# Performance work log

Hardware: AMD Instinct MI355X
Metric: run time of the kernel (lower is better)

Reference implementation:

```python
import jax, jax.numpy as jnp
import numpy as np

VS = 0.4
PC = (-75.2, -75.2, -2.0, 75.2, 75.2, 4.0)
K = 32            # max_points_per_voxel (stage 1)
K2 = 5            # max_points_per_voxel (stage 2)
MAXV = 50000      # max_num_voxels
GAMMA = 1.1
SENT = 1_000_000  # coord sentinel for empty voxel slots


def _voxelize(pts, valid, vx, vy, vz, max_vox, max_ppv):
    """Fixed-capacity voxelization (mimics spconv PointToVoxel).
    pts: [N,F] (xyz in first 3 cols); valid: [N] bool.
    Returns voxels [max_vox, max_ppv, F], coords_xy [max_vox,2] int32 (SENT for empty), num_points [max_vox]."""
    N, F = pts.shape
    gx = int(round((PC[3] - PC[0]) / vx))
    gy = int(round((PC[4] - PC[1]) / vy))
    gz = int(round((PC[5] - PC[2]) / vz))
    cx = jnp.floor((pts[:, 0] - PC[0]) / vx).astype(jnp.int32)
    cy = jnp.floor((pts[:, 1] - PC[1]) / vy).astype(jnp.int32)
    cz = jnp.floor((pts[:, 2] - PC[2]) / vz).astype(jnp.int32)
    inb = valid & (cx >= 0) & (cx < gx) & (cy >= 0) & (cy < gy) & (cz >= 0) & (cz < gz)
    BIG = gx * gy * gz
    vid = jnp.where(inb, (cz * gy + cy) * gx + cx, BIG)
    order = jnp.argsort(vid)  # stable sort groups points by voxel
    sid = vid[order]
    spts = pts[order]
    first = jnp.searchsorted(sid, sid, side='left')
    last = jnp.searchsorted(sid, sid, side='right')
    rank = jnp.arange(N, dtype=jnp.int32) - first.astype(jnp.int32)
    is_first = (rank == 0) & (sid < BIG)
    slot_all = jnp.cumsum(is_first.astype(jnp.int32)) - 1
    slot = slot_all[first]
    keep = (sid < BIG) & (rank < max_ppv) & (slot < max_vox)
    s = jnp.where(keep, slot, max_vox)
    r = jnp.where(keep, rank, 0)
    voxels = jnp.zeros((max_vox + 1, max_ppv, F), pts.dtype).at[s, r].set(spts)[:max_vox]
    sf = jnp.where(is_first & (slot_all < max_vox), slot_all, max_vox)
    cnt = jnp.where(is_first, jnp.minimum(last - first, max_ppv), 0).astype(jnp.int32)
    nump = jnp.zeros((max_vox + 1,), jnp.int32).at[sf].set(cnt)[:max_vox]
    cxy = jnp.stack([cx[order], cy[order]], -1)
    coords = jnp.full((max_vox + 1, 2), SENT, jnp.int32).at[sf].set(cxy)[:max_vox]
    return voxels, coords, nump


def _forward(points, trajectory_rois, backward_rois, valid_length, batch_size, num_sample):
    B, T, R, _ = trajectory_rois.shape
    pc_start = jnp.array(PC[:2], jnp.float32)
    mixed_xy = (trajectory_rois[..., :2] + backward_rois[..., :2]) * 0.5
    rois_xy = jnp.where(valid_length[..., None], mixed_xy, backward_rois[..., :2])
    rois = jnp.concatenate([rois_xy, backward_rois[..., 2:]], -1)
    per_batch = []
    for bs in range(B):
        per_frame = []
        for t in range(T):
            valid = (points[:, 0] == bs) & (jnp.abs(points[:, 5] - t * 0.1) < 0.001)
            pts = points[:, 1:6]  # (x,y,z,feat,time) = 5 point features
            boxes = rois[bs, t]   # [R,7]
            # ---- stage 1: coarse voxelization (full z column) ----
            vox, coords, nump = _voxelize(pts, valid, VS, VS, PC[5] - PC[2], MAXV, K)
            q = jnp.floor((boxes[:, :2] - pc_start) / VS)
            rad = jnp.ceil(jnp.linalg.norm(boxes[:, 3:5] / 2, axis=-1) * GAMMA / VS)
            dist = jnp.abs(q[:, None, :] - coords[None].astype(jnp.float32))  # [R,V,2]
            vmask = jnp.any(jnp.all(dist < rad[:, None, None], -1), 0)        # [V]
            npm = jnp.where(vmask, nump, 0)
            kvalid = (jnp.arange(K)[None, :] < npm[:, None]).reshape(-1)
            kpts = vox.reshape(-1, 5)
            # ---- stage 2: fine voxelization of key points ----
            vox1, coords1, _ = _voxelize(kpts, kvalid, VS / 2, VS / 2, VS / 2, MAXV, K2)
            q1 = jnp.floor((boxes[:, :2] - pc_start) / (VS / 2))
            dist1 = jnp.abs(q1[:, None, :] - coords1[None].astype(jnp.float32))  # [R,V1,2]
            vmask1 = jnp.all(dist1 < (rad * 2)[:, None, None], -1)               # [R,V1]
            _, sidx = jax.lax.top_k(vmask1.astype(jnp.float32), num_sample)      # [R,S]
            sv = vox1[sidx]                                   # [R,S,K2,F]
            sv = sv.transpose(0, 2, 1, 3).reshape(R, K2 * num_sample, 5)
            cur_r = jnp.linalg.norm(boxes[:, 3:5] / 2, axis=-1) * GAMMA
            pm = ((sv[:, :, :2] - boxes[:, None, :2]) ** 2).sum(-1) < cur_r[:, None] ** 2
            pm = pm & (sv[:, :, 2] <= (boxes[:, 2] + boxes[:, 5] * 0.6)[:, None])
            smask, sidx2 = jax.lax.top_k(pm.astype(jnp.float32), num_sample)
            sp = jnp.take_along_axis(sv, sidx2[:, :, None], axis=1)  # [R,S,5]
            sp = jnp.where(smask[:, :, None] > 0, sp, 0.0)
            per_frame.append(sp)
        per_batch.append(jnp.stack(per_frame))  # [T,R,S,5]
    res = jnp.stack(per_batch)                   # [B,T,R,S,5]
    return res.transpose(0, 2, 1, 3, 4).reshape(B, R, T * num_sample, 5)


def setup_inputs() -> dict:
    key = jax.random.key(0)
    k = jax.random.split(key, 10)
    N, B, T, R = 240000, 2, 4, 128
    bs = jax.random.randint(k[0], (N,), 0, B).astype(jnp.float32)
    frame = jax.random.randint(k[1], (N,), 0, T).astype(jnp.float32)
    x = jax.random.uniform(k[2], (N,), minval=-74.0, maxval=74.0)
    y = jax.random.uniform(k[3], (N,), minval=-74.0, maxval=74.0)
    z = jax.random.uniform(k[4], (N,), minval=-2.0, maxval=4.0)
    inten = jax.random.uniform(k[5], (N,))
    points = jnp.stack([bs, x, y, z, inten, frame * 0.1], -1)
    xy = jax.random.uniform(k[6], (B, T, R, 2), minval=-60.0, maxval=60.0)
    zc = jax.random.uniform(k[7], (B, T, R, 1), minval=-1.0, maxval=1.0)
    dims = jax.random.uniform(k[8], (B, T, R, 3), minval=1.0, maxval=5.0)
    yaw = jax.random.uniform(k[9], (B, T, R, 1), minval=-3.14, maxval=3.14)
    trajectory_rois = jnp.concatenate([xy, zc, dims, yaw], -1)
    backward_rois = trajectory_rois.at[..., :2].add(
        0.5 * jax.random.normal(jax.random.fold_in(key, 1), (B, T, R, 2)))
    valid_length = jax.random.randint(jax.random.fold_in(key, 2), (B, T, R), 0, 2).astype(bool)
    return {"points": points, "trajectory_rois": trajectory_rois,
            "backward_rois": backward_rois, "valid_length": valid_length,
            "batch_size": 2, "num_sample": 32}


def reference(points, trajectory_rois, backward_rois, valid_length, batch_size, num_sample):
    return _forward(points, trajectory_rois, backward_rois, valid_length, batch_size, num_sample)
```

## Files before the change

### kernel.cpp

```cpp
#include <hip/hip_runtime.h>

typedef unsigned int u32;
typedef unsigned long long u64;

#define BB 2
#define TT 4
#define NF 8
#define RR 128
#define NSAMP 32
#define KK2 5
#define GX1 376
#define GY1 376
#define GX2 752
#define GY2 752
#define GZ2 30
#define WPF 530160
#define RBW 12
#define NMAXP 262144
#define MAXROWS 1536
#define RPT 6
#define HCAP (1u << 19)
#define HMASK (HCAP - 1u)
#define EMPTYW 0xFFFFFFFFu
#define NOVID 0xFFFFFFFFu
#define NLOW 64
#define CW 8

#define PCX (-75.2f)
#define PCY (-75.2f)
#define PCZ (-2.0f)
#define VS1 0.4f
#define VSH 0.2f
#define VZ1 6.0f

__global__ void k_init(const float* traj, const float* back, const unsigned char* vlb,
                       u32* boxp, u32* z0, u32 n0, u32* f2, u32 n2)
{
    u32 tid = blockIdx.x * blockDim.x + threadIdx.x;
    u32 stride = gridDim.x * blockDim.x;
    if (tid < NF * RR) {
        int i = (int)tid;
        bool isU8 = false;
        for (int k = 1; k < 64; k++)
            if ((k & 3) && vlb[k]) isU8 = true;
        bool vl = isU8 ? (vlb[i] != 0) : (((const int*)vlb)[i] != 0);
        const float* tb = traj + i * 7;
        const float* bb = back + i * 7;
        float bx = vl ? (tb[0] + bb[0]) * 0.5f : bb[0];
        float by = vl ? (tb[1] + bb[1]) * 0.5f : bb[1];
        float bz = bb[2], dx = bb[3], dy = bb[4], dz = bb[5];
        float hx = dx * 0.5f, hy = dy * 0.5f;
        float r0 = sqrtf(hx * hx + hy * hy);
        float radf = ceilf(r0 * 1.1f / 0.4f);
        float curr = r0 * 1.1f;
        u32* bp = boxp + i * 12;
        bp[0] = __float_as_uint(bx);
        bp[1] = __float_as_uint(by);
        bp[2] = __float_as_uint(curr * curr);
        bp[3] = __float_as_uint(bz + dz * 0.6f);
        bp[4] = (u32)(int)floorf((bx - PCX) / VS1);
        bp[5] = (u32)(int)floorf((by - PCY) / VS1);
        bp[6] = (u32)(int)radf;
        bp[7] = (u32)(int)floorf((bx - PCX) / VSH);
        bp[8] = (u32)(int)floorf((by - PCY) / VSH);
        bp[9] = (u32)(2 * (int)radf);
    }
    uint4 zz = make_uint4(0u, 0u, 0u, 0u);
    uint4 fv = make_uint4(~0u, ~0u, ~0u, ~0u);
    for (u32 i = tid; i < n0; i += stride) ((uint4*)z0)[i] = zz;
    for (u32 i = tid; i < n2; i += stride) ((uint4*)f2)[i] = fv;
}

__global__ void k_raster(const u32* boxp, u32* roibm)
{
    int tid = blockIdx.x * blockDim.x + threadIdx.x;
    if (tid >= NF * RR) return;
    const u32* bp = boxp + tid * 12;
    int f = tid / RR;
    int Qx = (int)bp[4], Qy = (int)bp[5], ir = (int)bp[6];
    int xlo = Qx - ir + 1; if (xlo < 0) xlo = 0;
    int xhi = Qx + ir - 1; if (xhi > GX1 - 1) xhi = GX1 - 1;
    int ylo = Qy - ir + 1; if (ylo < 0) ylo = 0;
    int yhi = Qy + ir - 1; if (yhi > GY1 - 1) yhi = GY1 - 1;
    if (xlo > xhi || ylo > yhi) return;
    int w0 = xlo >> 5, w1 = xhi >> 5;
    for (int cy = ylo; cy <= yhi; cy++) {
        u32* row = roibm + (size_t)f * (GY1 * RBW) + cy * RBW;
        for (int w = w0; w <= w1; w++) {
            int lo = xlo - (w << 5); if (lo < 0) lo = 0;
            int hi = xhi - (w << 5); if (hi > 31) hi = 31;
            u32 m = (hi == 31 ? 0xFFFFFFFFu : ((1u << (hi + 1)) - 1u)) & ~((1u << lo) - 1u);
            atomicOr(&row[w], m);
        }
    }
}

__global__ void k_keep(const float* P, int n, const u32* roibm,
                       u32* bitmap, u32* tabk, u32* tabs)
{
    int i = blockIdx.x * blockDim.x + threadIdx.x;
    if (i >= n) return;
    const float* p = P + (size_t)i * 6;
    float bsf = p[0], x = p[1], y = p[2], z = p[3], tt = p[5];
    int b = (int)bsf;
    int t = (int)floorf(tt * 10.0f + 0.5f);
    if (!(bsf == (float)b && b >= 0 && b < BB && t >= 0 && t < TT &&
          fabsf(tt - 0.1f * (float)t) < 0.001f)) return;
    float fx = floorf((x - PCX) / VS1);
    float fy = floorf((y - PCY) / VS1);
    float fz = floorf((z - PCZ) / VZ1);
    if (!(fx >= 0.f && fx < (float)GX1 && fy >= 0.f && fy < (float)GY1 && fz == 0.f)) return;
    u32 f = (u32)(b * TT + t);
    u32 cx = (u32)fx, cy = (u32)fy;
    u32 bit = (roibm[(size_t)f * (GY1 * RBW) + cy * RBW + (cx >> 5)] >> (cx & 31)) & 1u;
    if (!bit) return;
    float fx2 = floorf((x - PCX) / VSH);
    float fy2 = floorf((y - PCY) / VSH);
    float fz2 = floorf((z - PCZ) / VSH);
    if (!(fx2 >= 0.f && fx2 < (float)GX2 && fy2 >= 0.f && fy2 < (float)GY2 &&
          fz2 >= 0.f && fz2 < (float)GZ2)) return;
    u32 vid = ((u32)fz2 * GY2 + (u32)fy2) * GX2 + (u32)fx2;
    u32 pk = (f << 25) | vid;
    atomicOr(&bitmap[f * WPF + (vid >> 5)], 1u << (vid & 31));
    u32 idx = ((pk * 2654435761u) >> 13) & HMASK;
    while (true) {
        u32 old = atomicCAS(&tabk[idx], EMPTYW, pk);
        if (old == EMPTYW || old == pk) break;
        idx = (idx + 1u) & HMASK;
    }
    u32* arr = tabs + (size_t)idx * KK2;
    u32 val = (u32)i;
    #pragma unroll
    for (int j = 0; j < KK2; j++) {
        u32 old = atomicMin(&arr[j], val);
        if (old == EMPTYW) break;
        val = old > val ? old : val;
    }
}

__global__ void __launch_bounds__(256) k_lowvid(const u32* bitmap, u32* lowvids)
{
    __shared__ u32 out_sh[NLOW];
    __shared__ u32 cnt_sh;
    __shared__ u32 wsum_sh[4];
    int f = blockIdx.x, tid = threadIdx.x;
    int lane = tid & 63, wid = tid >> 6;
    const u32* bmf = bitmap + (size_t)f * WPF;
    if (tid == 0) cnt_sh = 0;
    __syncthreads();
    for (u32 base = 0; base < (u32)WPF; base += 256 * CW) {
        u32 w[CW];
        u32 pc = 0;
        u32 tb = base + (u32)tid * CW;
        if (tb + CW <= (u32)WPF) {
            uint4 a = *(const uint4*)(bmf + tb);
            uint4 c4 = *(const uint4*)(bmf + tb + 4);
            w[0] = a.x; w[1] = a.y; w[2] = a.z; w[3] = a.w;
            w[4] = c4.x; w[5] = c4.y; w[6] = c4.z; w[7] = c4.w;
        } else {
            #pragma unroll
            for (u32 e = 0; e < CW; e++) w[e] = (tb + e < (u32)WPF) ? bmf[tb + e] : 0u;
        }
        #pragma unroll
        for (u32 e = 0; e < CW; e++) pc += (u32)__popc(w[e]);
        u32 ws = pc;
        #pragma unroll
        for (int off = 1; off < 64; off <<= 1) {
            u32 y = __shfl_up(ws, off, 64);
            if (lane >= off) ws += y;
        }
        if (lane == 63) wsum_sh[wid] = ws;
        __syncthreads();
        u32 w0 = wsum_sh[0], w1 = wsum_sh[1], w2 = wsum_sh[2], w3 = wsum_sh[3];
        u32 wexcl = (wid > 0 ? w0 : 0u) + (wid > 1 ? w1 : 0u) + (wid > 2 ? w2 : 0u);
        u32 excl = cnt_sh + wexcl + ws - pc;
        u32 totadd = w0 + w1 + w2 + w3;
        if (excl < NLOW && pc) {
            u32 c = excl;
            #pragma unroll
            for (u32 e = 0; e < CW; e++) {
                u32 ww = w[e];
                while (ww && c < NLOW) {
                    u32 b = (u32)__ffs(ww) - 1u;
                    out_sh[c++] = ((tb + e) << 5) | b;
                    ww &= ww - 1u;
                }
            }
        }
        __syncthreads();
        if (tid == 0) {
            u32 nc = cnt_sh + totadd;
            cnt_sh = nc > (u32)NLOW ? (u32)NLOW : nc;
        }
        __syncthreads();
        if (cnt_sh >= (u32)NLOW) break;
    }
    u32 c = cnt_sh;
    for (int e = tid; e < NLOW; e += 256)
        lowvids[f * NLOW + e] = ((u32)e < c) ? out_sh[e] : NOVID;
}

__global__ void __launch_bounds__(256) k_output(const float* P, const u32* boxp,
    const u32* bitmap, const u32* lowvids, const u32* tabk, const u32* tabs, float* out)
{
    __shared__ u32 rpref_s[MAXROWS];
    __shared__ u32 ssum[256];
    __shared__ u32 sidx[NSAMP];
    __shared__ float feat[KK2 * NSAMP][5];
    __shared__ u32 pmf[KK2 * NSAMP];
    __shared__ int sel[NSAMP];
    __shared__ int nsel_s;
    __shared__ u32 M_s;

    int bid = blockIdx.x, tid = threadIdx.x;
    int f = bid / RR, r = bid % RR;
    int b = f / TT, t = f % TT;
    const u32* bp = boxp + bid * 12;
    float bx = __uint_as_float(bp[0]);
    float by = __uint_as_float(bp[1]);
    float cr2 = __uint_as_float(bp[2]);
    float zmax = __uint_as_float(bp[3]);
    int Q1x = (int)bp[7], Q1y = (int)bp[8], irad2 = (int)bp[9];

    const u32* bmf = bitmap + (size_t)f * WPF;

    int cxlo = Q1x - irad2 + 1; if (cxlo < 0) cxlo = 0;
    int cxhi = Q1x + irad2 - 1; if (cxhi > GX2 - 1) cxhi = GX2 - 1;
    int cylo = Q1y - irad2 + 1; if (cylo < 0) cylo = 0;
    int cyhi = Q1y + irad2 - 1; if (cyhi > GY2 - 1) cyhi = GY2 - 1;
    int ny = cyhi - cylo + 1;
    int nrows = (cxlo <= cxhi && cylo <= cyhi) ? GZ2 * ny : 0;
    if (nrows > MAXROWS) nrows = MAXROWS;

    u32 myrpref[RPT];
    u32 lsum = 0;
    #pragma unroll
    for (int e = 0; e < RPT; e++) {
        int ri = tid * RPT + e;
        myrpref[e] = lsum;
        if (ri < nrows) {
            int cz = ri / ny, cy = cylo + (ri - cz * ny);
            u32 vlo = ((u32)cz * GY2 + (u32)cy) * GX2 + (u32)cxlo;
            u32 vhi = vlo + (u32)(cxhi - cxlo);
            u32 gwlo = vlo >> 5, gwhi = vhi >> 5;
            u32 c = 0;
            for (u32 gw = gwlo; gw <= gwhi; gw++) {
                u32 w = bmf[gw];
                u32 lob = (gw == gwlo) ? (vlo & 31u) : 0u;
                u32 hib = (gw == gwhi) ? (vhi & 31u) : 31u;
                u32 m = (hib == 31u ? 0xFFFFFFFFu : ((1u << (hib + 1)) - 1u)) & ~((1u << lob) - 1u);
                c += (u32)__popc(w & m);
            }
            lsum += c;
        }
    }
    ssum[tid] = lsum;
    __syncthreads();
    for (int off = 1; off < 256; off <<= 1) {
        u32 y = (tid >= off) ? ssum[tid - off] : 0;
        __syncthreads();
        ssum[tid] += y;
        __syncthreads();
    }
    u32 texcl = ssum[tid] - lsum;
    if (tid == 255) M_s = ssum[255];
    #pragma unroll
    for (int e = 0; e < RPT; e++) {
        int ri = tid * RPT + e;
        if (ri < MAXROWS) rpref_s[ri] = texcl + myrpref[e];
    }
    __syncthreads();

    u32 M = M_s;
    int nt = (int)(M < (u32)NSAMP ? M : (u32)NSAMP);
    if (tid < nt) {
        int lo = 0, hi = nrows - 1;
        while (lo < hi) { int m = (lo + hi + 1) >> 1; if (rpref_s[m] <= (u32)tid) lo = m; else hi = m - 1; }
        u32 rem = (u32)tid - rpref_s[lo];
        int cz = lo / ny, cy = cylo + (lo - cz * ny);
        u32 vlo = ((u32)cz * GY2 + (u32)cy) * GX2 + (u32)cxlo;
        u32 vhi = vlo + (u32)(cxhi - cxlo);
        u32 gwlo = vlo >> 5, gwhi = vhi >> 5;
        u32 vsel = NOVID;
        for (u32 gw = gwlo; gw <= gwhi; gw++) {
            u32 w = bmf[gw];
            u32 lob = (gw == gwlo) ? (vlo & 31u) : 0u;
            u32 hib = (gw == gwhi) ? (vhi & 31u) : 31u;
            u32 m = (hib == 31u ? 0xFFFFFFFFu : ((1u << (hib + 1)) - 1u)) & ~((1u << lob) - 1u);
            u32 wm = w & m;
            u32 pc = (u32)__popc(wm);
            if (rem < pc) {
                for (u32 k = 0; k < rem; k++) wm &= wm - 1u;
                u32 bit = (u32)__ffs(wm) - 1u;
                vsel = (gw << 5) | bit;
                break;
            }
            rem -= pc;
        }
        sidx[tid] = vsel;
    }
    __syncthreads();
    if (tid == 0) {
        const u32* lv = lowvids + f * NLOW;
        int c = nt, p = 0, q = 0;
        while (c < NSAMP) {
            u32 cand = (q < NLOW) ? lv[q] : NOVID;
            if (cand == NOVID) { sidx[c++] = NOVID; continue; }
            if (p < nt && sidx[p] == cand) { p++; q++; continue; }
            sidx[c++] = cand; q++;
        }
    }
    __syncthreads();

    for (int j2 = tid; j2 < KK2 * NSAMP; j2 += 256) {
        int s = j2 / KK2, k2 = j2 - s * KK2;
        int j = k2 * NSAMP + s;
        u32 vid = sidx[s];
        float px = 0.f, py = 0.f, pz = 0.f, pi = 0.f, pt = 0.f;
        if (vid != NOVID) {
            u32 pk = ((u32)f << 25) | vid;
            u32 idx = ((pk * 2654435761u) >> 13) & HMASK;
            u32 key;
            while (true) {
                key = tabk[idx];
                if (key == pk || key == EMPTYW) break;
                idx = (idx + 1u) & HMASK;
            }
            if (key == pk) {
                u32 pidx = tabs[(size_t)idx * KK2 + k2];
                if (pidx != EMPTYW) {
                    const float* p = P + (size_t)pidx * 6;
                    px = p[1]; py = p[2]; pz = p[3]; pi = p[4]; pt = p[5];
                }
            }
        }
        feat[j][0] = px; feat[j][1] = py; feat[j][2] = pz; feat[j][3] = pi; feat[j][4] = pt;
        float ex = px - bx, ey = py - by;
        pmf[j] = (ex * ex + ey * ey < cr2 && pz <= zmax) ? 1u : 0u;
    }
    __syncthreads();

    if (tid == 0) {
        int c = 0;
        for (int j = 0; j < KK2 * NSAMP && c < NSAMP; j++)
            if (pmf[j]) sel[c++] = j;
        nsel_s = c;
    }
    __syncthreads();

    int obase = ((b * RR + r) * (TT * NSAMP) + t * NSAMP) * 5;
    for (int w = tid; w < NSAMP * 5; w += 256) {
        int row = w / 5, col = w % 5;
        float v = (row < nsel_s) ? feat[sel[row]][col] : 0.f;
        out[obase + w] = v;
    }
}

extern "C" void kernel_launch(void* const* d_in, const int* in_sizes, int n_in,
                              void* d_out, int out_size, void* d_ws, size_t ws_size,
                              hipStream_t stream)
{
    const float* P = (const float*)d_in[0];
    const float* traj = (const float*)d_in[1];
    const float* back = (const float*)d_in[2];
    const unsigned char* vlb = (const unsigned char*)d_in[3];
    float* out = (float*)d_out;
    int N = in_sizes[0] / 6;
    if (N > NMAXP) N = NMAXP;

    char* cur = (char*)d_ws;
    auto carve = [&](size_t bytes) -> char* {
        char* p = cur;
        cur += (bytes + 255) & ~(size_t)255;
        return p;
    };

    char* zoneZ = cur;
    u32* roibm  = (u32*)carve((size_t)NF * GY1 * RBW * 4);
    u32* bitmap = (u32*)carve((size_t)NF * WPF * 4);
    size_t z_bytes = (size_t)(cur - zoneZ);
    u32* tabk = (u32*)carve((size_t)HCAP * 4);
    u32* tabs = (u32*)carve((size_t)HCAP * KK2 * 4);
    size_t ff_bytes = (size_t)(cur - (char*)tabk);

    u32* boxp    = (u32*)carve((size_t)NF * RR * 12 * 4);
    u32* lowvids = (u32*)carve((size_t)NF * NLOW * 4);
    if ((size_t)(cur - (char*)d_ws) > ws_size) return;

    k_init<<<1024, 256, 0, stream>>>(traj, back, vlb, boxp,
                                     (u32*)zoneZ, (u32)(z_bytes / 16),
                                     tabk, (u32)(ff_bytes / 16));

    k_raster<<<(NF * RR + 255) / 256, 256, 0, stream>>>(boxp, roibm);

    k_keep<<<(N + 255) / 256, 256, 0, stream>>>(P, N, roibm, bitmap, tabk, tabs);

    k_lowvid<<<NF, 256, 0, stream>>>(bitmap, lowvids);

    k_output<<<NF * RR, 256, 0, stream>>>(P, boxp, bitmap, lowvids, tabk, tabs, out);
}
```

Baseline: 70.07 us.

## Fuse ROI rasterization into init kernel, use wave-shuffle scans, widen lowvid chunk

Removes the separate k_raster launch. The ROI bitmap is now built inside k_init in gather form: each thread owns one bitmap word and ORs in masks from all 128 boxes of its frame, read from shared memory, so no atomics or zero-init of that bitmap are needed. The block prefix sum in k_output switches from a shared-memory Hillis-Steele scan with many barriers to a wave-shuffle scan plus a per-wave total. k_lowvid now loads 32 words per thread instead of 8. In exchange, k_init recomputes box parameters per block and each thread loops over all boxes.

```diff
diff --git a/kernel.cpp b/kernel.cpp
--- a/kernel.cpp
+++ b/kernel.cpp
@@ -16,6 +16,8 @@
 #define GZ2 30
 #define WPF 530160
 #define RBW 12
+#define RWPF 4512
+#define RPB 18
 #define NMAXP 262144
 #define MAXROWS 1536
 #define RPT 6
@@ -24,7 +26,7 @@
 #define EMPTYW 0xFFFFFFFFu
 #define NOVID 0xFFFFFFFFu
 #define NLOW 64
-#define CW 8
+#define CW 32
 
 #define PCX (-75.2f)
 #define PCY (-75.2f)
@@ -33,13 +35,15 @@
 #define VSH 0.2f
 #define VZ1 6.0f
 
-__global__ void k_init(const float* traj, const float* back, const unsigned char* vlb,
-                       u32* boxp, u32* z0, u32 n0, u32* f2, u32 n2)
+__global__ void __launch_bounds__(256) k_init(const float* traj, const float* back,
+                                              const unsigned char* vlb, u32* boxp, u32* roibm,
+                                              u32* z0, u32 n0, u32* f2, u32 n2)
 {
-    u32 tid = blockIdx.x * blockDim.x + threadIdx.x;
-    u32 stride = gridDim.x * blockDim.x;
-    if (tid < NF * RR) {
-        int i = (int)tid;
+    u32 bid = blockIdx.x, tid = threadIdx.x;
+    u32 gtid = bid * 256 + tid;
+    u32 stride = gridDim.x * 256;
+    if (gtid < NF * RR) {
+        int i = (int)gtid;
         bool isU8 = false;
         for (int k = 1; k < 64; k++)
             if ((k & 3) && vlb[k]) isU8 = true;
@@ -65,34 +69,54 @@
         bp[8] = (u32)(int)floorf((by - PCY) / VSH);
         bp[9] = (u32)(2 * (int)radf);
     }
+    if (bid < NF * RPB) {
+        __shared__ int qx_s[RR], qy_s[RR], ir_s[RR];
+        int f = (int)bid / RPB, j = (int)bid % RPB;
+        if (tid < RR) {
+            int i = f * RR + (int)tid;
+            bool isU8 = false;
+            for (int k = 1; k < 64; k++)
+                if ((k & 3) && vlb[k]) isU8 = true;
+            bool vl = isU8 ? (vlb[i] != 0) : (((const int*)vlb)[i] != 0);
+            const float* tb = traj + i * 7;
+            const float* bb = back + i * 7;
+            float bx = vl ? (tb[0] + bb[0]) * 0.5f : bb[0];
+            float by = vl ? (tb[1] + bb[1]) * 0.5f : bb[1];
+            float dx = bb[3], dy = bb[4];
+            float hx = dx * 0.5f, hy = dy * 0.5f;
+            float r0 = sqrtf(hx * hx + hy * hy);
+            qx_s[tid] = (int)floorf((bx - PCX) / VS1);
+            qy_s[tid] = (int)floorf((by - PCY) / VS1);
+            ir_s[tid] = (int)ceilf(r0 * 1.1f / 0.4f);
+        }
+        __syncthreads();
+        int w = j * 256 + (int)tid;
+        if (w < RWPF) {
+            int cy = w / RBW, wj = w - cy * RBW;
+            int xw0 = wj << 5;
+            u32 acc = 0;
+            #pragma unroll 4
+            for (int r = 0; r < RR; r++) {
+                int ir = ir_s[r];
+                int dyv = cy - qy_s[r];
+                if (dyv >= ir || dyv <= -ir) continue;
+                int Qx = qx_s[r];
+                int xlo = Qx - ir + 1; if (xlo < 0) xlo = 0;
+                int xhi = Qx + ir - 1; if (xhi > GX1 - 1) xhi = GX1 - 1;
+                if (xlo > xhi) continue;
+                int lo = xlo - xw0, hi = xhi - xw0;
+                if (hi < 0 || lo > 31) continue;
+                if (lo < 0) lo = 0;
+                if (hi > 31) hi = 31;
+                acc |= (hi == 31 ? 0xFFFFFFFFu : ((1u << (hi + 1)) - 1u)) & ~((1u << lo) - 1u);
+            }
+            roibm[(size_t)f * RWPF + w] = acc;
+        }
+    }
     uint4 zz = make_uint4(0u, 0u, 0u, 0u);
     uint4 fv = make_uint4(~0u, ~0u, ~0u, ~0u);
-    for (u32 i = tid; i < n0; i += stride) ((uint4*)z0)[i] = zz;
-    for (u32 i = tid; i < n2; i += stride) ((uint4*)f2)[i] = fv;
-}
-
-__global__ void k_raster(const u32* boxp, u32* roibm)
-{
-    int tid = blockIdx.x * blockDim.x + threadIdx.x;
-    if (tid >= NF * RR) return;
-    const u32* bp = boxp + tid * 12;
-    int f = tid / RR;
-    int Qx = (int)bp[4], Qy = (int)bp[5], ir = (int)bp[6];
-    int xlo = Qx - ir + 1; if (xlo < 0) xlo = 0;
-    int xhi = Qx + ir - 1; if (xhi > GX1 - 1) xhi = GX1 - 1;
-    int ylo = Qy - ir + 1; if (ylo < 0) ylo = 0;
-    int yhi = Qy + ir - 1; if (yhi > GY1 - 1) yhi = GY1 - 1;
-    if (xlo > xhi || ylo > yhi) return;
-    int w0 = xlo >> 5, w1 = xhi >> 5;
-    for (int cy = ylo; cy <= yhi; cy++) {
-        u32* row = roibm + (size_t)f * (GY1 * RBW) + cy * RBW;
-        for (int w = w0; w <= w1; w++) {
-            int lo = xlo - (w << 5); if (lo < 0) lo = 0;
-            int hi = xhi - (w << 5); if (hi > 31) hi = 31;
-            u32 m = (hi == 31 ? 0xFFFFFFFFu : ((1u << (hi + 1)) - 1u)) & ~((1u << lo) - 1u);
-            atomicOr(&row[w], m);
-        }
-    }
+    for (u32 i = gtid; i < n0; i += stride) ((uint4*)z0)[i] = zz;
+    for (u32 i = gtid; i < n2; i += stride) ((uint4*)f2)[i] = fv;
 }
 
 __global__ void k_keep(const float* P, int n, const u32* roibm,
@@ -112,7 +136,7 @@
     if (!(fx >= 0.f && fx < (float)GX1 && fy >= 0.f && fy < (float)GY1 && fz == 0.f)) return;
     u32 f = (u32)(b * TT + t);
     u32 cx = (u32)fx, cy = (u32)fy;
-    u32 bit = (roibm[(size_t)f * (GY1 * RBW) + cy * RBW + (cx >> 5)] >> (cx & 31)) & 1u;
+    u32 bit = (roibm[(size_t)f * RWPF + cy * RBW + (cx >> 5)] >> (cx & 31)) & 1u;
     if (!bit) return;
     float fx2 = floorf((x - PCX) / VSH);
     float fy2 = floorf((y - PCY) / VSH);
@@ -153,10 +177,11 @@
         u32 pc = 0;
         u32 tb = base + (u32)tid * CW;
         if (tb + CW <= (u32)WPF) {
-            uint4 a = *(const uint4*)(bmf + tb);
-            uint4 c4 = *(const uint4*)(bmf + tb + 4);
-            w[0] = a.x; w[1] = a.y; w[2] = a.z; w[3] = a.w;
-            w[4] = c4.x; w[5] = c4.y; w[6] = c4.z; w[7] = c4.w;
+            #pragma unroll
+            for (u32 q = 0; q < CW / 4; q++) {
+                uint4 a = *(const uint4*)(bmf + tb + q * 4);
+                w[q * 4 + 0] = a.x; w[q * 4 + 1] = a.y; w[q * 4 + 2] = a.z; w[q * 4 + 3] = a.w;
+            }
         } else {
             #pragma unroll
             for (u32 e = 0; e < CW; e++) w[e] = (tb + e < (u32)WPF) ? bmf[tb + e] : 0u;
@@ -204,15 +229,15 @@
     const u32* bitmap, const u32* lowvids, const u32* tabk, const u32* tabs, float* out)
 {
     __shared__ u32 rpref_s[MAXROWS];
-    __shared__ u32 ssum[256];
+    __shared__ u32 wsum_sh[4];
     __shared__ u32 sidx[NSAMP];
     __shared__ float feat[KK2 * NSAMP][5];
     __shared__ u32 pmf[KK2 * NSAMP];
     __shared__ int sel[NSAMP];
     __shared__ int nsel_s;
-    __shared__ u32 M_s;
 
     int bid = blockIdx.x, tid = threadIdx.x;
+    int lane = tid & 63, wid = tid >> 6;
     int f = bid / RR, r = bid % RR;
     int b = f / TT, t = f % TT;
     const u32* bp = boxp + bid * 12;
@@ -254,16 +279,18 @@
             lsum += c;
         }
     }
-    ssum[tid] = lsum;
-    __syncthreads();
-    for (int off = 1; off < 256; off <<= 1) {
-        u32 y = (tid >= off) ? ssum[tid - off] : 0;
-        __syncthreads();
-        ssum[tid] += y;
-        __syncthreads();
-    }
-    u32 texcl = ssum[tid] - lsum;
-    if (tid == 255) M_s = ssum[255];
+    u32 ws = lsum;
+    #pragma unroll
+    for (int off = 1; off < 64; off <<= 1) {
+        u32 y = __shfl_up(ws, off, 64);
+        if (lane >= off) ws += y;
+    }
+    if (lane == 63) wsum_sh[wid] = ws;
+    __syncthreads();
+    u32 w0 = wsum_sh[0], w1 = wsum_sh[1], w2 = wsum_sh[2], w3 = wsum_sh[3];
+    u32 wexcl = (wid > 0 ? w0 : 0u) + (wid > 1 ? w1 : 0u) + (wid > 2 ? w2 : 0u);
+    u32 texcl = wexcl + ws - lsum;
+    u32 M = w0 + w1 + w2 + w3;
     #pragma unroll
     for (int e = 0; e < RPT; e++) {
         int ri = tid * RPT + e;
@@ -271,7 +298,6 @@
     }
     __syncthreads();
 
-    u32 M = M_s;
     int nt = (int)(M < (u32)NSAMP ? M : (u32)NSAMP);
     if (tid < nt) {
         int lo = 0, hi = nrows - 1;
@@ -375,23 +401,20 @@
         return p;
     };
 
-    char* zoneZ = cur;
-    u32* roibm  = (u32*)carve((size_t)NF * GY1 * RBW * 4);
     u32* bitmap = (u32*)carve((size_t)NF * WPF * 4);
-    size_t z_bytes = (size_t)(cur - zoneZ);
+    size_t z_bytes = (size_t)NF * WPF * 4;
     u32* tabk = (u32*)carve((size_t)HCAP * 4);
     u32* tabs = (u32*)carve((size_t)HCAP * KK2 * 4);
     size_t ff_bytes = (size_t)(cur - (char*)tabk);
 
+    u32* roibm   = (u32*)carve((size_t)NF * RWPF * 4);
     u32* boxp    = (u32*)carve((size_t)NF * RR * 12 * 4);
     u32* lowvids = (u32*)carve((size_t)NF * NLOW * 4);
     if ((size_t)(cur - (char*)d_ws) > ws_size) return;
 
-    k_init<<<1024, 256, 0, stream>>>(traj, back, vlb, boxp,
-                                     (u32*)zoneZ, (u32)(z_bytes / 16),
+    k_init<<<1024, 256, 0, stream>>>(traj, back, vlb, boxp, roibm,
+                                     bitmap, (u32)(z_bytes / 16),
                                      tabk, (u32)(ff_bytes / 16));
-
-    k_raster<<<(NF * RR + 255) / 256, 256, 0, stream>>>(boxp, roibm);
 
     k_keep<<<(N + 255) / 256, 256, 0, stream>>>(P, N, roibm, bitmap, tabk, tabs);
 
```

New measurement: 75.83 us. +8.2%, slower.
